# Kernel optimization log

Hardware: AMD Instinct MI355X
Metric: run time of the kernel (lower is better)

## Reference

```python
import jax, jax.numpy as jnp
import numpy as np

SOBEL_X = jnp.array([[1., 0., -1.], [2., 0., -2.], [1., 0., -1.]], dtype=jnp.float32).reshape(1, 1, 3, 3)
SOBEL_Y = jnp.array([[1., 2., 1.], [0., 0., 0.], [-1., -2., -1.]], dtype=jnp.float32).reshape(1, 1, 3, 3)
EPS = 1e-3


def _sobel(img, kern):
    # img: [N, 1, H, W]; 3x3 conv, zero padding 1 (torch Conv2d padding=1)
    return jax.lax.conv_general_dilated(
        img, kern, window_strides=(1, 1), padding='SAME',
        dimension_numbers=('NCHW', 'OIHW', 'NCHW'))


def _compute_flow(frames):
    # frames: [B, T, 3, H, W] -> flow: [B, T-1, 2, H, W]
    B, T, C, H, W = frames.shape
    gray = (0.2989 * frames[:, :, 0] + 0.587 * frames[:, :, 1]
            + 0.114 * frames[:, :, 2])  # [B, T, H, W]
    I1 = gray[:, :-1].reshape(B * (T - 1), 1, H, W)
    I2 = gray[:, 1:].reshape(B * (T - 1), 1, H, W)
    Ix = _sobel(I1, SOBEL_X)
    Iy = _sobel(I1, SOBEL_Y)
    It = I2 - I1
    denom = Ix * Ix + Iy * Iy + EPS
    u = -Ix * It / denom
    v = -Iy * It / denom
    return jnp.concatenate([u, v], axis=1).reshape(B, T - 1, 2, H, W)


def setup_inputs() -> dict:
    key = jax.random.key(0)
    k1, k2 = jax.random.split(key)
    shape = (8, 8, 3, 256, 256)  # [B, T, C, H, W]
    pred = jax.random.uniform(k1, shape, dtype=jnp.float32)
    gt = jax.random.uniform(k2, shape, dtype=jnp.float32)
    return {"pred": pred, "gt": gt}


def reference(pred, gt):
    pred_flow = _compute_flow(pred)  # [B, T-1, 2, H, W]
    gt_flow = _compute_flow(gt)
    # motion magnitude: mean abs frame diff over channels, broadcast over 2 flow channels
    motion_mag = jnp.abs(gt[:, 1:] - gt[:, :-1]).mean(axis=2, keepdims=True)  # [B, T-1, 1, H, W]
    flow_loss = (jnp.abs(pred_flow - gt_flow) * motion_mag).mean()
    return flow_loss
```

## Files before the change

kernel.cpp:

```cpp
#include <hip/hip_runtime.h>

#define BB 8
#define TT 8
#define HH 256
#define WW 256
#define FRAME_PIX (HH * WW)
#define RROWS 8
#define PADW 264
#define NY (HH / RROWS)
#define NBLK (BB * 2 * NY)
#define EPS 1e-3f
#define INV_N (1.0f / (float)((size_t)BB * (TT - 1) * 2 * HH * WW))

__device__ __forceinline__ float4 ld4(const float* __restrict__ p) {
    return *reinterpret_cast<const float4*>(p);
}

__device__ __forceinline__ float4 gray4(const float4 r, const float4 g, const float4 b) {
    float4 o;
    o.x = 0.2989f * r.x + 0.587f * g.x + 0.114f * b.x;
    o.y = 0.2989f * r.y + 0.587f * g.y + 0.114f * b.y;
    o.z = 0.2989f * r.z + 0.587f * g.z + 0.114f * b.z;
    o.w = 0.2989f * r.w + 0.587f * g.w + 0.114f * b.w;
    return o;
}

__global__ __launch_bounds__(256, 2) void flow_loss_kernel(
    const float* __restrict__ pred, const float* __restrict__ gt,
    float* __restrict__ partial)
{
    __shared__ float gbuf[2][RROWS + 2][PADW];

    const int ytile = blockIdx.x;
    const int half  = blockIdx.y;
    const int b     = blockIdx.z;
    const int t0    = half * 4;
    const int npair = half ? 3 : 4;
    const int y0    = ytile * RROWS;
    const int tid   = threadIdx.x;
    const size_t fs = (size_t)3 * FRAME_PIX;
    const float* pb = pred + (size_t)b * TT * fs;
    const float* gb = gt   + (size_t)b * TT * fs;

    const int cx  = (tid & 63) * 4;
    const int rb_ = tid >> 6;

    const int h_img  = tid >> 7;
    const int h_rsel = (tid >> 6) & 1;
    const int h_x    = (tid & 63) * 4;
    const int h_y    = h_rsel ? (y0 + RROWS) : (y0 - 1);
    const bool h_ok  = ((unsigned)h_y) < HH;
    const int h_brow = h_rsel ? (RROWS + 1) : 0;
    const size_t h_off = h_ok ? ((size_t)h_y * WW + h_x) : 0;

    if (tid < 160) {
        const int img = tid / 80, rem = tid % 80, row = rem / 8, k = rem % 8;
        const int col = (k < 4) ? k : (k + 256);
        gbuf[img][row][col] = 0.f;
    }

    float4 g1c[2][3];

    {
        const float* p1 = pb + (size_t)t0 * fs;
        const float* g1 = gb + (size_t)t0 * fs;
        float4 pg[2], gg[2];
        #pragma unroll
        for (int pass = 0; pass < 2; ++pass) {
            const int r = pass * 4 + rb_;
            const size_t off = (size_t)(y0 + r) * WW + cx;
            const float4 pr = ld4(p1 + off), pgc = ld4(p1 + off + FRAME_PIX),
                         pbc = ld4(p1 + off + 2 * FRAME_PIX);
            g1c[pass][0] = ld4(g1 + off);
            g1c[pass][1] = ld4(g1 + off + FRAME_PIX);
            g1c[pass][2] = ld4(g1 + off + 2 * FRAME_PIX);
            pg[pass] = gray4(pr, pgc, pbc);
            gg[pass] = gray4(g1c[pass][0], g1c[pass][1], g1c[pass][2]);
        }
        const float* hb = h_img ? g1 : p1;
        float4 hg = make_float4(0.f, 0.f, 0.f, 0.f);
        if (h_ok) {
            const float4 r0 = ld4(hb + h_off), g0 = ld4(hb + h_off + FRAME_PIX),
                         b0 = ld4(hb + h_off + 2 * FRAME_PIX);
            hg = gray4(r0, g0, b0);
        }
        #pragma unroll
        for (int pass = 0; pass < 2; ++pass) {
            const int r = pass * 4 + rb_;
            *reinterpret_cast<float4*>(&gbuf[0][r + 1][cx + 4]) = pg[pass];
            *reinterpret_cast<float4*>(&gbuf[1][r + 1][cx + 4]) = gg[pass];
        }
        *reinterpret_cast<float4*>(&gbuf[h_img][h_brow][h_x + 4]) = hg;
    }
    __syncthreads();

    float s = 0.f;
    for (int t = t0; t < t0 + npair; ++t) {
        const float* p2 = pb + (size_t)(t + 1) * fs;
        const float* g2 = gb + (size_t)(t + 1) * fs;

        float4 p2c[2][3], g2c[2][3];
        #pragma unroll
        for (int pass = 0; pass < 2; ++pass) {
            const int r = pass * 4 + rb_;
            const size_t off = (size_t)(y0 + r) * WW + cx;
            p2c[pass][0] = ld4(p2 + off);
            p2c[pass][1] = ld4(p2 + off + FRAME_PIX);
            p2c[pass][2] = ld4(p2 + off + 2 * FRAME_PIX);
            g2c[pass][0] = ld4(g2 + off);
            g2c[pass][1] = ld4(g2 + off + FRAME_PIX);
            g2c[pass][2] = ld4(g2 + off + 2 * FRAME_PIX);
        }
        const float* hb = h_img ? g2 : p2;
        float4 hgray = make_float4(0.f, 0.f, 0.f, 0.f);
        if (h_ok) {
            const float4 r0 = ld4(hb + h_off), g0 = ld4(hb + h_off + FRAME_PIX),
                         b0 = ld4(hb + h_off + 2 * FRAME_PIX);
            hgray = gray4(r0, g0, b0);
        }

        float4 gp2[2], gg2[2];
        #pragma unroll
        for (int pass = 0; pass < 2; ++pass) {
            gp2[pass] = gray4(p2c[pass][0], p2c[pass][1], p2c[pass][2]);
            gg2[pass] = gray4(g2c[pass][0], g2c[pass][1], g2c[pass][2]);
        }

        #pragma unroll
        for (int pass = 0; pass < 2; ++pass) {
            const int r = pass * 4 + rb_;
            float mm[4];
            mm[0] = (fabsf(g2c[pass][0].x - g1c[pass][0].x) + fabsf(g2c[pass][1].x - g1c[pass][1].x)
                   + fabsf(g2c[pass][2].x - g1c[pass][2].x)) * (1.f / 3.f);
            mm[1] = (fabsf(g2c[pass][0].y - g1c[pass][0].y) + fabsf(g2c[pass][1].y - g1c[pass][1].y)
                   + fabsf(g2c[pass][2].y - g1c[pass][2].y)) * (1.f / 3.f);
            mm[2] = (fabsf(g2c[pass][0].z - g1c[pass][0].z) + fabsf(g2c[pass][1].z - g1c[pass][1].z)
                   + fabsf(g2c[pass][2].z - g1c[pass][2].z)) * (1.f / 3.f);
            mm[3] = (fabsf(g2c[pass][0].w - g1c[pass][0].w) + fabsf(g2c[pass][1].w - g1c[pass][1].w)
                   + fabsf(g2c[pass][2].w - g1c[pass][2].w)) * (1.f / 3.f);

            float up[4], vp[4];
            #pragma unroll
            for (int img = 0; img < 2; ++img) {
                float w0[6], w1[6], w2[6];
                {
                    const float* p = &gbuf[img][r][cx];
                    const float4 A = ld4(p), B = ld4(p + 4), C = ld4(p + 8);
                    w0[0] = A.w; w0[1] = B.x; w0[2] = B.y; w0[3] = B.z; w0[4] = B.w; w0[5] = C.x;
                }
                {
                    const float* p = &gbuf[img][r + 1][cx];
                    const float4 A = ld4(p), B = ld4(p + 4), C = ld4(p + 8);
                    w1[0] = A.w; w1[1] = B.x; w1[2] = B.y; w1[3] = B.z; w1[4] = B.w; w1[5] = C.x;
                }
                {
                    const float* p = &gbuf[img][r + 2][cx];
                    const float4 A = ld4(p), B = ld4(p + 4), C = ld4(p + 8);
                    w2[0] = A.w; w2[1] = B.x; w2[2] = B.y; w2[3] = B.z; w2[4] = B.w; w2[5] = C.x;
                }
                const float4 gr2 = img ? gg2[pass] : gp2[pass];
                const float g2a[4] = {gr2.x, gr2.y, gr2.z, gr2.w};
                #pragma unroll
                for (int j = 0; j < 4; ++j) {
                    const float Ix = (w0[j] - w0[j + 2]) + 2.0f * (w1[j] - w1[j + 2]) + (w2[j] - w2[j + 2]);
                    const float Iy = (w0[j] + 2.0f * w0[j + 1] + w0[j + 2])
                                   - (w2[j] + 2.0f * w2[j + 1] + w2[j + 2]);
                    const float It = g2a[j] - w1[j + 1];
                    const float inv = 1.0f / (Ix * Ix + Iy * Iy + EPS);
                    if (img == 0) {
                        up[j] = -(Ix * It) * inv;
                        vp[j] = -(Iy * It) * inv;
                    } else {
                        s += (fabsf(up[j] + (Ix * It) * inv) + fabsf(vp[j] + (Iy * It) * inv)) * mm[j];
                    }
                }
            }
        }
        __syncthreads();

        #pragma unroll
        for (int pass = 0; pass < 2; ++pass) {
            const int r = pass * 4 + rb_;
            *reinterpret_cast<float4*>(&gbuf[0][r + 1][cx + 4]) = gp2[pass];
            *reinterpret_cast<float4*>(&gbuf[1][r + 1][cx + 4]) = gg2[pass];
            g1c[pass][0] = g2c[pass][0];
            g1c[pass][1] = g2c[pass][1];
            g1c[pass][2] = g2c[pass][2];
        }
        *reinterpret_cast<float4*>(&gbuf[h_img][h_brow][h_x + 4]) = hgray;
        __syncthreads();
    }

    #pragma unroll
    for (int off = 32; off > 0; off >>= 1) s += __shfl_down(s, off, 64);

    __shared__ float wsum[4];
    if ((tid & 63) == 0) wsum[tid >> 6] = s;
    __syncthreads();
    if (tid == 0) {
        partial[(b * 2 + half) * NY + ytile] = wsum[0] + wsum[1] + wsum[2] + wsum[3];
    }
}

__global__ __launch_bounds__(256) void reduce_kernel(
    const float* __restrict__ partial, float* __restrict__ out)
{
    float s = partial[threadIdx.x] + partial[threadIdx.x + 256];
    #pragma unroll
    for (int off = 32; off > 0; off >>= 1) s += __shfl_down(s, off, 64);

    __shared__ float wsum[4];
    if ((threadIdx.x & 63) == 0) wsum[threadIdx.x >> 6] = s;
    __syncthreads();
    if (threadIdx.x == 0) {
        out[0] = (wsum[0] + wsum[1] + wsum[2] + wsum[3]) * INV_N;
    }
}

extern "C" void kernel_launch(void* const* d_in, const int* in_sizes, int n_in,
                              void* d_out, int out_size, void* d_ws, size_t ws_size,
                              hipStream_t stream) {
    const float* pred = (const float*)d_in[0];
    const float* gt   = (const float*)d_in[1];
    float* partial    = (float*)d_ws;
    float* out        = (float*)d_out;

    dim3 grid(NY, 2, BB);
    dim3 block(256);
    flow_loss_kernel<<<grid, block, 0, stream>>>(pred, gt, partial);
    reduce_kernel<<<1, 256, 0, stream>>>(partial, out);
}
```

Before: 122.1 us.

## Split tiles along x, prefetch the next frame in registers, raise occupancy

Each 8-row tile is split into two 128-column x-tiles, doubling the grid to 1024 blocks with one float4 per thread per row. Left and right halo columns are now loaded explicitly by extra threads. The loads for frame t+2 are issued before the Sobel and flow math on frame t+1, so global memory latency overlaps with compute, and the motion magnitude is computed a step ahead. Launch bounds are raised to 4 blocks per SM. The costs are extra halo traffic at the x seams and more registers spent holding the prefetched values.

After: 121.0 us. Within noise of the previous version (-0.9%).

```diff
diff --git a/kernel.cpp b/kernel.cpp
--- a/kernel.cpp
+++ b/kernel.cpp
@@ -5,17 +5,21 @@
 #define HH 256
 #define WW 256
 #define FRAME_PIX (HH * WW)
+#define XW 128
 #define RROWS 8
-#define PADW 264
-#define NY (HH / RROWS)
-#define NBLK (BB * 2 * NY)
+#define NYT (HH / RROWS)
+#define NXT (WW / XW)
+#define PADW 136
+#define NBLK (BB * 2 * NYT * NXT)
 #define EPS 1e-3f
 #define INV_N (1.0f / (float)((size_t)BB * (TT - 1) * 2 * HH * WW))
 
 __device__ __forceinline__ float4 ld4(const float* __restrict__ p) {
     return *reinterpret_cast<const float4*>(p);
 }
-
+__device__ __forceinline__ void st4(float* p, const float4 v) {
+    *reinterpret_cast<float4*>(p) = v;
+}
 __device__ __forceinline__ float4 gray4(const float4 r, const float4 g, const float4 b) {
     float4 o;
     o.x = 0.2989f * r.x + 0.587f * g.x + 0.114f * b.x;
@@ -25,170 +29,183 @@
     return o;
 }
 
-__global__ __launch_bounds__(256, 2) void flow_loss_kernel(
+__global__ __launch_bounds__(256, 4) void flow_loss_kernel(
     const float* __restrict__ pred, const float* __restrict__ gt,
     float* __restrict__ partial)
 {
     __shared__ float gbuf[2][RROWS + 2][PADW];
 
-    const int ytile = blockIdx.x;
+    const int ytile = blockIdx.x >> 1;
+    const int xtile = blockIdx.x & 1;
     const int half  = blockIdx.y;
     const int b     = blockIdx.z;
     const int t0    = half * 4;
-    const int npair = half ? 3 : 4;
+    const int tend  = t0 + (half ? 3 : 4);
     const int y0    = ytile * RROWS;
+    const int x0    = xtile * XW;
     const int tid   = threadIdx.x;
     const size_t fs = (size_t)3 * FRAME_PIX;
     const float* pb = pred + (size_t)b * TT * fs;
     const float* gb = gt   + (size_t)b * TT * fs;
 
-    const int cx  = (tid & 63) * 4;
-    const int rb_ = tid >> 6;
-
-    const int h_img  = tid >> 7;
-    const int h_rsel = (tid >> 6) & 1;
-    const int h_x    = (tid & 63) * 4;
-    const int h_y    = h_rsel ? (y0 + RROWS) : (y0 - 1);
-    const bool h_ok  = ((unsigned)h_y) < HH;
-    const int h_brow = h_rsel ? (RROWS + 1) : 0;
-    const size_t h_off = h_ok ? ((size_t)h_y * WW + h_x) : 0;
-
-    if (tid < 160) {
-        const int img = tid / 80, rem = tid % 80, row = rem / 8, k = rem % 8;
-        const int col = (k < 4) ? k : (k + 256);
-        gbuf[img][row][col] = 0.f;
-    }
-
-    float4 g1c[2][3];
+    const int r  = tid >> 5;
+    const int cx = (tid & 31) * 4;
+    const size_t coff = (size_t)(y0 + r) * WW + (x0 + cx);
+
+    bool e_act = false, e_val = false;
+    int  e_img = 0;
+    size_t e_off = 0;
+    float* e_dst = &gbuf[0][0][0];
+    if (tid < 128) {
+        e_act = true;
+        e_img = tid >> 6;
+        const int rsel = (tid >> 5) & 1;
+        const int ec   = (tid & 31) * 4;
+        const int ey   = rsel ? (y0 + RROWS) : (y0 - 1);
+        e_val = (unsigned)ey < HH;
+        e_off = e_val ? ((size_t)ey * WW + x0 + ec) : 0;
+        e_dst = &gbuf[e_img][rsel ? RROWS + 1 : 0][4 + ec];
+    } else if (tid < 168) {
+        const int j = tid - 128;
+        e_act = true;
+        e_img = j / 20;
+        const int rem  = j % 20;
+        const int side = rem / 10;
+        const int prow = rem % 10;
+        const int ey = y0 - 1 + prow;
+        const int ex = side ? (x0 + XW) : (x0 - 4);
+        e_val = ((unsigned)ey < HH) && ((unsigned)ex < WW);
+        e_off = e_val ? ((size_t)ey * WW + ex) : 0;
+        e_dst = &gbuf[e_img][prow][side ? 4 + XW : 0];
+    }
+
+    float4 p2c[3], g2c[3], ecur[3];
+    float  mmc[4];
 
     {
         const float* p1 = pb + (size_t)t0 * fs;
         const float* g1 = gb + (size_t)t0 * fs;
-        float4 pg[2], gg[2];
+        const float4 pr  = ld4(p1 + coff);
+        const float4 pg  = ld4(p1 + coff + FRAME_PIX);
+        const float4 pbl = ld4(p1 + coff + 2 * FRAME_PIX);
+        const float4 a0  = ld4(g1 + coff);
+        const float4 a1  = ld4(g1 + coff + FRAME_PIX);
+        const float4 a2  = ld4(g1 + coff + 2 * FRAME_PIX);
+        const float* eb0 = e_img ? g1 : p1;
+        float4 x0v = make_float4(0.f,0.f,0.f,0.f), x1v = x0v, x2v = x0v;
+        if (e_act && e_val) {
+            x0v = ld4(eb0 + e_off);
+            x1v = ld4(eb0 + e_off + FRAME_PIX);
+            x2v = ld4(eb0 + e_off + 2 * FRAME_PIX);
+        }
+        const float* p2 = p1 + fs;
+        const float* g2 = g1 + fs;
+        p2c[0] = ld4(p2 + coff);
+        p2c[1] = ld4(p2 + coff + FRAME_PIX);
+        p2c[2] = ld4(p2 + coff + 2 * FRAME_PIX);
+        g2c[0] = ld4(g2 + coff);
+        g2c[1] = ld4(g2 + coff + FRAME_PIX);
+        g2c[2] = ld4(g2 + coff + 2 * FRAME_PIX);
+        const float* eb1 = e_img ? g2 : p2;
+        ecur[0] = make_float4(0.f,0.f,0.f,0.f); ecur[1] = ecur[0]; ecur[2] = ecur[0];
+        if (e_act && e_val) {
+            ecur[0] = ld4(eb1 + e_off);
+            ecur[1] = ld4(eb1 + e_off + FRAME_PIX);
+            ecur[2] = ld4(eb1 + e_off + 2 * FRAME_PIX);
+        }
+        st4(&gbuf[0][r + 1][4 + cx], gray4(pr, pg, pbl));
+        st4(&gbuf[1][r + 1][4 + cx], gray4(a0, a1, a2));
+        if (e_act) st4(e_dst, gray4(x0v, x1v, x2v));
+        mmc[0] = (fabsf(g2c[0].x - a0.x) + fabsf(g2c[1].x - a1.x) + fabsf(g2c[2].x - a2.x)) * (1.f/3.f);
+        mmc[1] = (fabsf(g2c[0].y - a0.y) + fabsf(g2c[1].y - a1.y) + fabsf(g2c[2].y - a2.y)) * (1.f/3.f);
+        mmc[2] = (fabsf(g2c[0].z - a0.z) + fabsf(g2c[1].z - a1.z) + fabsf(g2c[2].z - a2.z)) * (1.f/3.f);
+        mmc[3] = (fabsf(g2c[0].w - a0.w) + fabsf(g2c[1].w - a1.w) + fabsf(g2c[2].w - a2.w)) * (1.f/3.f);
+    }
+    __syncthreads();
+
+    float s = 0.f;
+    for (int t = t0; t < tend; ++t) {
+        const bool more = (t + 1 < tend);
+
+        float4 p2n[3], g2n[3], en[3];
+        if (more) {
+            const float* p3 = pb + (size_t)(t + 2) * fs;
+            const float* g3 = gb + (size_t)(t + 2) * fs;
+            p2n[0] = ld4(p3 + coff);
+            p2n[1] = ld4(p3 + coff + FRAME_PIX);
+            p2n[2] = ld4(p3 + coff + 2 * FRAME_PIX);
+            g2n[0] = ld4(g3 + coff);
+            g2n[1] = ld4(g3 + coff + FRAME_PIX);
+            g2n[2] = ld4(g3 + coff + 2 * FRAME_PIX);
+            const float* eb = e_img ? g3 : p3;
+            en[0] = make_float4(0.f,0.f,0.f,0.f); en[1] = en[0]; en[2] = en[0];
+            if (e_act && e_val) {
+                en[0] = ld4(eb + e_off);
+                en[1] = ld4(eb + e_off + FRAME_PIX);
+                en[2] = ld4(eb + e_off + 2 * FRAME_PIX);
+            }
+        }
+
+        const float4 gp2 = gray4(p2c[0], p2c[1], p2c[2]);
+        const float4 gg2 = gray4(g2c[0], g2c[1], g2c[2]);
+
+        float up[4], vp[4];
         #pragma unroll
-        for (int pass = 0; pass < 2; ++pass) {
-            const int r = pass * 4 + rb_;
-            const size_t off = (size_t)(y0 + r) * WW + cx;
-            const float4 pr = ld4(p1 + off), pgc = ld4(p1 + off + FRAME_PIX),
-                         pbc = ld4(p1 + off + 2 * FRAME_PIX);
-            g1c[pass][0] = ld4(g1 + off);
-            g1c[pass][1] = ld4(g1 + off + FRAME_PIX);
-            g1c[pass][2] = ld4(g1 + off + 2 * FRAME_PIX);
-            pg[pass] = gray4(pr, pgc, pbc);
-            gg[pass] = gray4(g1c[pass][0], g1c[pass][1], g1c[pass][2]);
-        }
-        const float* hb = h_img ? g1 : p1;
-        float4 hg = make_float4(0.f, 0.f, 0.f, 0.f);
-        if (h_ok) {
-            const float4 r0 = ld4(hb + h_off), g0 = ld4(hb + h_off + FRAME_PIX),
-                         b0 = ld4(hb + h_off + 2 * FRAME_PIX);
-            hg = gray4(r0, g0, b0);
-        }
-        #pragma unroll
-        for (int pass = 0; pass < 2; ++pass) {
-            const int r = pass * 4 + rb_;
-            *reinterpret_cast<float4*>(&gbuf[0][r + 1][cx + 4]) = pg[pass];
-            *reinterpret_cast<float4*>(&gbuf[1][r + 1][cx + 4]) = gg[pass];
-        }
-        *reinterpret_cast<float4*>(&gbuf[h_img][h_brow][h_x + 4]) = hg;
-    }
-    __syncthreads();
-
-    float s = 0.f;
-    for (int t = t0; t < t0 + npair; ++t) {
-        const float* p2 = pb + (size_t)(t + 1) * fs;
-        const float* g2 = gb + (size_t)(t + 1) * fs;
-
-        float4 p2c[2][3], g2c[2][3];
-        #pragma unroll
-        for (int pass = 0; pass < 2; ++pass) {
-            const int r = pass * 4 + rb_;
-            const size_t off = (size_t)(y0 + r) * WW + cx;
-            p2c[pass][0] = ld4(p2 + off);
-            p2c[pass][1] = ld4(p2 + off + FRAME_PIX);
-            p2c[pass][2] = ld4(p2 + off + 2 * FRAME_PIX);
-            g2c[pass][0] = ld4(g2 + off);
-            g2c[pass][1] = ld4(g2 + off + FRAME_PIX);
-            g2c[pass][2] = ld4(g2 + off + 2 * FRAME_PIX);
-        }
-        const float* hb = h_img ? g2 : p2;
-        float4 hgray = make_float4(0.f, 0.f, 0.f, 0.f);
-        if (h_ok) {
-            const float4 r0 = ld4(hb + h_off), g0 = ld4(hb + h_off + FRAME_PIX),
-                         b0 = ld4(hb + h_off + 2 * FRAME_PIX);
-            hgray = gray4(r0, g0, b0);
-        }
-
-        float4 gp2[2], gg2[2];
-        #pragma unroll
-        for (int pass = 0; pass < 2; ++pass) {
-            gp2[pass] = gray4(p2c[pass][0], p2c[pass][1], p2c[pass][2]);
-            gg2[pass] = gray4(g2c[pass][0], g2c[pass][1], g2c[pass][2]);
-        }
-
-        #pragma unroll
-        for (int pass = 0; pass < 2; ++pass) {
-            const int r = pass * 4 + rb_;
-            float mm[4];
-            mm[0] = (fabsf(g2c[pass][0].x - g1c[pass][0].x) + fabsf(g2c[pass][1].x - g1c[pass][1].x)
-                   + fabsf(g2c[pass][2].x - g1c[pass][2].x)) * (1.f / 3.f);
-            mm[1] = (fabsf(g2c[pass][0].y - g1c[pass][0].y) + fabsf(g2c[pass][1].y - g1c[pass][1].y)
-                   + fabsf(g2c[pass][2].y - g1c[pass][2].y)) * (1.f / 3.f);
-            mm[2] = (fabsf(g2c[pass][0].z - g1c[pass][0].z) + fabsf(g2c[pass][1].z - g1c[pass][1].z)
-                   + fabsf(g2c[pass][2].z - g1c[pass][2].z)) * (1.f / 3.f);
-            mm[3] = (fabsf(g2c[pass][0].w - g1c[pass][0].w) + fabsf(g2c[pass][1].w - g1c[pass][1].w)
-                   + fabsf(g2c[pass][2].w - g1c[pass][2].w)) * (1.f / 3.f);
-
-            float up[4], vp[4];
+        for (int img = 0; img < 2; ++img) {
+            float w0[6], w1[6], w2[6];
+            {
+                const float* p = &gbuf[img][r][cx];
+                const float4 A = ld4(p), B = ld4(p + 4), C = ld4(p + 8);
+                w0[0] = A.w; w0[1] = B.x; w0[2] = B.y; w0[3] = B.z; w0[4] = B.w; w0[5] = C.x;
+            }
+            {
+                const float* p = &gbuf[img][r + 1][cx];
+                const float4 A = ld4(p), B = ld4(p + 4), C = ld4(p + 8);
+                w1[0] = A.w; w1[1] = B.x; w1[2] = B.y; w1[3] = B.z; w1[4] = B.w; w1[5] = C.x;
+            }
+            {
+                const float* p = &gbuf[img][r + 2][cx];
+                const float4 A = ld4(p), B = ld4(p + 4), C = ld4(p + 8);
+                w2[0] = A.w; w2[1] = B.x; w2[2] = B.y; w2[3] = B.z; w2[4] = B.w; w2[5] = C.x;
+            }
+            const float4 gr2 = img ? gg2 : gp2;
+            const float g2a[4] = {gr2.x, gr2.y, gr2.z, gr2.w};
             #pragma unroll
-            for (int img = 0; img < 2; ++img) {
-                float w0[6], w1[6], w2[6];
-                {
-                    const float* p = &gbuf[img][r][cx];
-                    const float4 A = ld4(p), B = ld4(p + 4), C = ld4(p + 8);
-                    w0[0] = A.w; w0[1] = B.x; w0[2] = B.y; w0[3] = B.z; w0[4] = B.w; w0[5] = C.x;
+            for (int j = 0; j < 4; ++j) {
+                const float Ix = (w0[j] - w0[j + 2]) + 2.0f * (w1[j] - w1[j + 2]) + (w2[j] - w2[j + 2]);
+                const float Iy = (w0[j] + 2.0f * w0[j + 1] + w0[j + 2])
+                               - (w2[j] + 2.0f * w2[j + 1] + w2[j + 2]);
+                const float It = g2a[j] - w1[j + 1];
+                const float inv = 1.0f / (Ix * Ix + Iy * Iy + EPS);
+                if (img == 0) {
+                    up[j] = -(Ix * It) * inv;
+                    vp[j] = -(Iy * It) * inv;
+                } else {
+                    s += (fabsf(up[j] + (Ix * It) * inv) + fabsf(vp[j] + (Iy * It) * inv)) * mmc[j];
                 }
-                {
-                    const float* p = &gbuf[img][r + 1][cx];
-                    const float4 A = ld4(p), B = ld4(p + 4), C = ld4(p + 8);
-                    w1[0] = A.w; w1[1] = B.x; w1[2] = B.y; w1[3] = B.z; w1[4] = B.w; w1[5] = C.x;
-                }
-                {
-                    const float* p = &gbuf[img][r + 2][cx];
-                    const float4 A = ld4(p), B = ld4(p + 4), C = ld4(p + 8);
-                    w2[0] = A.w; w2[1] = B.x; w2[2] = B.y; w2[3] = B.z; w2[4] = B.w; w2[5] = C.x;
-                }
-                const float4 gr2 = img ? gg2[pass] : gp2[pass];
-                const float g2a[4] = {gr2.x, gr2.y, gr2.z, gr2.w};
-                #pragma unroll
-                for (int j = 0; j < 4; ++j) {
-                    const float Ix = (w0[j] - w0[j + 2]) + 2.0f * (w1[j] - w1[j + 2]) + (w2[j] - w2[j + 2]);
-                    const float Iy = (w0[j] + 2.0f * w0[j + 1] + w0[j + 2])
-                                   - (w2[j] + 2.0f * w2[j + 1] + w2[j + 2]);
-                    const float It = g2a[j] - w1[j + 1];
-                    const float inv = 1.0f / (Ix * Ix + Iy * Iy + EPS);
-                    if (img == 0) {
-                        up[j] = -(Ix * It) * inv;
-                        vp[j] = -(Iy * It) * inv;
-                    } else {
-                        s += (fabsf(up[j] + (Ix * It) * inv) + fabsf(vp[j] + (Iy * It) * inv)) * mm[j];
-                    }
-                }
-            }
-        }
-        __syncthreads();
-
-        #pragma unroll
-        for (int pass = 0; pass < 2; ++pass) {
-            const int r = pass * 4 + rb_;
-            *reinterpret_cast<float4*>(&gbuf[0][r + 1][cx + 4]) = gp2[pass];
-            *reinterpret_cast<float4*>(&gbuf[1][r + 1][cx + 4]) = gg2[pass];
-            g1c[pass][0] = g2c[pass][0];
-            g1c[pass][1] = g2c[pass][1];
-            g1c[pass][2] = g2c[pass][2];
-        }
-        *reinterpret_cast<float4*>(&gbuf[h_img][h_brow][h_x + 4]) = hgray;
-        __syncthreads();
+            }
+        }
+
+        if (more) {
+            float mmn[4];
+            mmn[0] = (fabsf(g2n[0].x - g2c[0].x) + fabsf(g2n[1].x - g2c[1].x) + fabsf(g2n[2].x - g2c[2].x)) * (1.f/3.f);
+            mmn[1] = (fabsf(g2n[0].y - g2c[0].y) + fabsf(g2n[1].y - g2c[1].y) + fabsf(g2n[2].y - g2c[2].y)) * (1.f/3.f);
+            mmn[2] = (fabsf(g2n[0].z - g2c[0].z) + fabsf(g2n[1].z - g2c[1].z) + fabsf(g2n[2].z - g2c[2].z)) * (1.f/3.f);
+            mmn[3] = (fabsf(g2n[0].w - g2c[0].w) + fabsf(g2n[1].w - g2c[1].w) + fabsf(g2n[2].w - g2c[2].w)) * (1.f/3.f);
+
+            __syncthreads();
+            st4(&gbuf[0][r + 1][4 + cx], gp2);
+            st4(&gbuf[1][r + 1][4 + cx], gg2);
+            if (e_act) st4(e_dst, gray4(ecur[0], ecur[1], ecur[2]));
+            #pragma unroll
+            for (int k = 0; k < 3; ++k) {
+                p2c[k] = p2n[k];
+                g2c[k] = g2n[k];
+                ecur[k] = en[k];
+            }
+            mmc[0] = mmn[0]; mmc[1] = mmn[1]; mmc[2] = mmn[2]; mmc[3] = mmn[3];
+            __syncthreads();
+        }
     }
 
     #pragma unroll
@@ -198,14 +215,16 @@
     if ((tid & 63) == 0) wsum[tid >> 6] = s;
     __syncthreads();
     if (tid == 0) {
-        partial[(b * 2 + half) * NY + ytile] = wsum[0] + wsum[1] + wsum[2] + wsum[3];
+        partial[(b * 2 + half) * (NYT * NXT) + blockIdx.x] =
+            wsum[0] + wsum[1] + wsum[2] + wsum[3];
     }
 }
 
 __global__ __launch_bounds__(256) void reduce_kernel(
     const float* __restrict__ partial, float* __restrict__ out)
 {
-    float s = partial[threadIdx.x] + partial[threadIdx.x + 256];
+    const float4 v = ld4(partial + threadIdx.x * 4);
+    float s = (v.x + v.y) + (v.z + v.w);
     #pragma unroll
     for (int off = 32; off > 0; off >>= 1) s += __shfl_down(s, off, 64);
 
@@ -225,7 +244,7 @@
     float* partial    = (float*)d_ws;
     float* out        = (float*)d_out;
 
-    dim3 grid(NY, 2, BB);
+    dim3 grid(NYT * NXT, 2, BB);
     dim3 block(256);
     flow_loss_kernel<<<grid, block, 0, stream>>>(pred, gt, partial);
     reduce_kernel<<<1, 256, 0, stream>>>(partial, out);
```
